# Kernel tuning notes

Measured on AMD Instinct MI355X. Metric: run time of the kernel, lower is better.

Reference implementation:

```python
import jax, jax.numpy as jnp
from jax import lax
import numpy as np


def gen_position(p, pos_decay=1.0):
    # Fixed relative-position bias: (9, p*p), neighbor order di*3+dj
    ar = jnp.arange(p, dtype=jnp.float32)
    right = jnp.broadcast_to(jnp.exp(-ar / (p / pos_decay))[None, :], (p, p))  # decays along width
    down = right.T                                                             # decays along height
    i, j = jnp.meshgrid(ar, ar, indexing='ij')
    br = jnp.exp(-(i + j) / (p / pos_decay))
    ones = jnp.ones((p, p), jnp.float32)
    merge = jnp.stack([
        jnp.rot90(br, 2), down[::-1, :], jnp.rot90(br, 1),
        right[:, ::-1], ones, right,
        jnp.rot90(br, 3), down, br,
    ], axis=0)
    return merge.reshape(9, -1)


def attention_conv(x, w_qkv, b_qkv, head_w, window_size, num_heads):
    b, c, h, w = x.shape
    p = window_size // 3
    pad_h = (p * (1 + h // p) - h) % p
    pad_w = (p * (1 + w // p) - w) % p
    xp = jnp.pad(x, ((0, 0), (0, 0), (p + pad_h, p), (p + pad_w, p)), mode='reflect')
    Hp, Wp = xp.shape[2], xp.shape[3]
    nH, nW = Hp // p - 2, Wp // p - 2  # == number of unfold windows (stride p, size 3p)
    # Non-overlapping p x p tiles; each window = 3x3 grid of adjacent tiles.
    tiles = xp.reshape(b, c, nH + 2, p, nW + 2, p).transpose(0, 2, 4, 1, 3, 5)  # [b,nH+2,nW+2,c,p,p]
    neigh = jnp.stack([tiles[:, di:di + nH, dj:dj + nW]
                       for di in range(3) for dj in range(3)], axis=3)  # [b,nH,nW,9,c,p,p]
    L = c * p * p
    pp = p * p
    xw = neigh.reshape(b * nH * nW, 9, L)
    qkv = xw @ w_qkv.T + b_qkv                                  # [N,9,nh*3*L]
    qkv = qkv.reshape(-1, 9, num_heads, 3, c, pp).transpose(0, 2, 4, 3, 1, 5)  # [N,nh,C,3,9,pp]
    q, k, v = qkv[:, :, :, 0], qkv[:, :, :, 1], qkv[:, :, :, 2]  # each [N,nh,C,9,pp]
    bias = gen_position(p)                                       # [9,pp]
    core_q = q[:, :, :, 4, :]                                    # center patch query [N,nh,C,pp]
    score = jnp.einsum('nhcp,nhckp->nhck', core_q, k * bias) / jnp.sqrt(jnp.float32(L))
    attn = jax.nn.softmax(score, axis=-1)                        # over 9 neighbors
    out = jnp.einsum('nhck,nhckp->nhcp', attn, v).reshape(-1, num_heads, L)
    out = jnp.einsum('h,nhd->nd', head_w[0], out)                # head mixing [N,L]
    out = out.reshape(b, nH, nW, c, p, p).transpose(0, 3, 1, 4, 2, 5).reshape(b, c, nH * p, nW * p)
    return out[:, :, pad_h:, pad_w:]


def setup_inputs() -> dict:
    key = jax.random.key(0)
    ks = jax.random.split(key, 8)
    B, C, H, W = 4, 3, 256, 256
    x = jax.random.uniform(ks[0], (B, C, H, W), dtype=jnp.float32)
    # conv3: window 3, p=1, heads 6, L=3 ; conv6: window 6, p=2, heads 4, L=12 ; conv9: window 9, p=3, heads 2, L=27
    w3_qkv = jax.random.normal(ks[1], (6 * 3 * 3, 3), jnp.float32) * 0.2
    b3_qkv = jnp.zeros((6 * 3 * 3,), jnp.float32)
    hw3 = jnp.full((1, 6), 1.0 / 6.0, jnp.float32)
    w6_qkv = jax.random.normal(ks[2], (4 * 3 * 12, 12), jnp.float32) * 0.1
    b6_qkv = jnp.zeros((4 * 3 * 12,), jnp.float32)
    hw6 = jnp.full((1, 4), 1.0 / 4.0, jnp.float32)
    w9_qkv = jax.random.normal(ks[3], (2 * 3 * 27, 27), jnp.float32) * 0.07
    b9_qkv = jnp.zeros((2 * 3 * 27,), jnp.float32)
    hw9 = jnp.full((1, 2), 1.0 / 2.0, jnp.float32)
    conv0_w = jax.random.normal(ks[4], (3, 9, 5, 5), jnp.float32) * 0.05
    conv0_b = jnp.zeros((3,), jnp.float32)
    return {"x": x, "w3_qkv": w3_qkv, "b3_qkv": b3_qkv, "hw3": hw3,
            "w6_qkv": w6_qkv, "b6_qkv": b6_qkv, "hw6": hw6,
            "w9_qkv": w9_qkv, "b9_qkv": b9_qkv, "hw9": hw9,
            "conv0_w": conv0_w, "conv0_b": conv0_b}


def reference(x, w3_qkv, b3_qkv, hw3, w6_qkv, b6_qkv, hw6,
              w9_qkv, b9_qkv, hw9, conv0_w, conv0_b):
    b, c, h, w = x.shape
    # global prior: softmax over size-1 dim (== ones), then global max pool
    gavg = jnp.mean((1.0 - x).reshape(b, c, -1), axis=-1, keepdims=True)       # [b,c,1]
    x_g = jax.nn.softmax(gavg, axis=-1)[..., None]                             # [b,c,1,1]
    x_g = jnp.max((x * x_g).reshape(b, 1, -1), axis=-1, keepdims=True)[..., None]  # [b,1,1,1]
    x3 = attention_conv(x,  w3_qkv, b3_qkv, hw3, 3, 6)
    x6 = attention_conv(x3, w6_qkv, b6_qkv, hw6, 6, 4)
    x9 = attention_conv(x6, w9_qkv, b9_qkv, hw9, 9, 2)
    cat = jnp.concatenate([x9, x6, x3], axis=1)                                # [b,9,h,w]
    x0 = jax.nn.relu(lax.conv_general_dilated(cat, conv0_w, (1, 1), ((2, 2), (2, 2)),
                                              dimension_numbers=('NCHW', 'OIHW', 'NCHW'))
                     + conv0_b[None, :, None, None])
    return jax.nn.relu(x * x0 + (x_g - x0))
```

## Files before the change

kernel.cpp:

```cpp
#include <hip/hip_runtime.h>
#include <math.h>

__device__ __forceinline__ int refl256(int t) {
    t = t < 0 ? -t : t;
    return t > 255 ? 510 - t : t;
}

__global__ __launch_bounds__(256)
void attn_p1v(const float* __restrict__ x, const float* __restrict__ w,
              const float* __restrict__ bq, const float* __restrict__ hw,
              float* __restrict__ out, float* __restrict__ pmax)
{
    int t = blockIdx.x * 256 + threadIdx.x;
    int xx = t & 255, yp = (t >> 8) & 127, bb = t >> 15;
    int y0 = yp * 2;
    const float* xb = x + bb * 196608;
    int rs[4], cs[3];
#pragma unroll
    for (int dr = 0; dr < 4; ++dr) rs[dr] = refl256(y0 + dr - 1) << 8;
#pragma unroll
    for (int dc = 0; dc < 3; ++dc) cs[dc] = refl256(xx + dc - 1);
    float xw[4][3][3];
#pragma unroll
    for (int dr = 0; dr < 4; ++dr)
#pragma unroll
        for (int dc = 0; dc < 3; ++dc)
#pragma unroll
            for (int c = 0; c < 3; ++c)
                xw[dr][dc][c] = xb[c * 65536 + rs[dr] + cs[dc]];

    {
        float bm = 0.f;
#pragma unroll
        for (int c = 0; c < 3; ++c)
            bm = fmaxf(bm, fmaxf(xw[1][1][c], xw[2][1][c]));
#pragma unroll
        for (int off = 32; off > 0; off >>= 1)
            bm = fmaxf(bm, __shfl_down(bm, off, 64));
        __shared__ float sm[4];
        int lane = threadIdx.x & 63, wid = threadIdx.x >> 6;
        if (lane == 0) sm[wid] = bm;
        __syncthreads();
        if (threadIdx.x == 0)
            pmax[blockIdx.x] = fmaxf(fmaxf(sm[0], sm[1]), fmaxf(sm[2], sm[3]));
    }

    float ov0[3] = {0.f, 0.f, 0.f}, ov1[3] = {0.f, 0.f, 0.f};
    const float scl = 0.57735026919f;
#pragma unroll 1
    for (int h = 0; h < 6; ++h) {
        float hwh = hw[h];
#pragma unroll
        for (int cc = 0; cc < 3; ++cc) {
            int oq = 9 * h + cc, ok = oq + 3, oV = oq + 6;
            float wq0 = w[oq * 3], wq1 = w[oq * 3 + 1], wq2 = w[oq * 3 + 2];
            float wk0 = w[ok * 3], wk1 = w[ok * 3 + 1], wk2 = w[ok * 3 + 2];
            float wv0 = w[oV * 3], wv1 = w[oV * 3 + 1], wv2 = w[oV * 3 + 2];
            float bk = bq[ok], bv = bq[oV];
            float kp[12], vp[12];
#pragma unroll
            for (int pos = 0; pos < 12; ++pos) {
                const float* xv = xw[pos / 3][pos % 3];
                kp[pos] = fmaf(xv[0], wk0, fmaf(xv[1], wk1, fmaf(xv[2], wk2, bk)));
                vp[pos] = fmaf(xv[0], wv0, fmaf(xv[1], wv1, fmaf(xv[2], wv2, bv)));
            }
            float q0 = fmaf(xw[1][1][0], wq0, fmaf(xw[1][1][1], wq1, fmaf(xw[1][1][2], wq2, bq[oq]))) * scl;
            float q1 = fmaf(xw[2][1][0], wq0, fmaf(xw[2][1][1], wq1, fmaf(xw[2][1][2], wq2, bq[oq]))) * scl;
            float se0 = 0.f, ac0 = 0.f, se1 = 0.f, ac1 = 0.f;
#pragma unroll
            for (int j = 0; j < 9; ++j) {
                float e0 = __expf(q0 * kp[j]);
                se0 += e0; ac0 = fmaf(e0, vp[j], ac0);
                float e1 = __expf(q1 * kp[3 + j]);
                se1 += e1; ac1 = fmaf(e1, vp[3 + j], ac1);
            }
            ov0[cc] = fmaf(hwh, ac0 / se0, ov0[cc]);
            ov1[cc] = fmaf(hwh, ac1 / se1, ov1[cc]);
        }
    }
    int pix = (y0 << 8) + xx;
    float* ob = out + bb * 196608;
#pragma unroll
    for (int cc = 0; cc < 3; ++cc) {
        ob[cc * 65536 + pix] = ov0[cc];
        ob[cc * 65536 + pix + 256] = ov1[cc];
    }
}

template<int P, int NH, int NWIN, int OFS, int GSU, int NCH>
__global__ __launch_bounds__(64 * NCH)
void proj2_pk(const float* __restrict__ x, const float* __restrict__ w,
              const float* __restrict__ bq, float* __restrict__ kv)
{
    constexpr int PP = P * P, L = 3 * PP, NO = NH * 9 * PP, NG = NO / GSU;
    constexpr int CPG = NG / NCH;
    constexpr int NT = NWIN + 2, T4 = 4 * NT * NT;
    constexpr int LR = (L & 1) ? L : L + 1;
    __shared__ float s_x[64 * LR];
    const int tid = threadIdx.y * 64 + threadIdx.x;
    const int t0 = blockIdx.x * 64;
    for (int idx = tid; idx < 64 * L; idx += 64 * NCH) {
        int lane = idx & 63, l = idx >> 6;
        int t = t0 + lane;
        if (t < T4) {
            int bb = t / (NT * NT), rr = t - bb * NT * NT;
            int ty = rr / NT, tx = rr - ty * NT;
            int c = l / PP, pos = l - c * PP;
            int i = pos / P, j = pos - i * P;
            int pr = refl256(ty * P + i - OFS);
            int pc = refl256(tx * P + j - OFS);
            s_x[lane * LR + l] = x[bb * 196608 + c * 65536 + (pr << 8) + pc];
        }
    }
    __syncthreads();
    const int t = t0 + threadIdx.x;
    if (t >= T4) return;
    const int chunk = __builtin_amdgcn_readfirstlane((int)threadIdx.y);
    float xw[L];
#pragma unroll
    for (int l = 0; l < L; ++l) xw[l] = s_x[threadIdx.x * LR + l];
    float4* dst = (float4*)kv + t + (size_t)chunk * CPG * T4;
#pragma unroll 1
    for (int g = 0; g < CPG; ++g) {
        int go = (chunk * CPG + g) * GSU;
        float acc[GSU];
#pragma unroll
        for (int e = 0; e < GSU; ++e) acc[e] = bq[go + e];
#pragma unroll
        for (int l = 0; l < L; ++l) {
            float xv = xw[l];
#pragma unroll
            for (int e = 0; e < GSU; ++e)
                acc[e] = fmaf(xv, w[(go + e) * L + l], acc[e]);
        }
        float4 o4;
        o4.x = acc[0];
        o4.y = acc[1];
        o4.z = acc[2];
        o4.w = (GSU == 4) ? acc[GSU - 1] : 0.f;
        dst[(size_t)g * T4] = o4;
    }
}

template<int P, int NH, int NWIN, int OFS, int GSU>
__global__ __launch_bounds__(256)
void attn2_pk(const float* __restrict__ kv, const float* __restrict__ hw,
              float* __restrict__ out)
{
    constexpr int PP = P * P, NT = NWIN + 2, T4 = 4 * NT * NT, PAD = OFS - P;
    constexpr int NGP = (PP + GSU - 1) / GSU;
    constexpr float SCL = (P == 2) ? 0.28867513459481287f : 0.19245008972987526f;
    __shared__ float s_bias[9 * PP];
    int tid = threadIdx.x;
    if (tid < 9 * PP) {
        int j = tid / PP, pos = tid - j * PP;
        int i = pos / P, jj = pos - i * P;
        int di = j / 3, dj = j - di * 3;
        float er = (di == 0) ? (float)(P - 1 - i) : (di == 2 ? (float)i : 0.f);
        float ec = (dj == 0) ? (float)(P - 1 - jj) : (dj == 2 ? (float)jj : 0.f);
        s_bias[tid] = __expf(-(er + ec) / (float)P);
    }
    __syncthreads();
    int wlin = blockIdx.x * 256 + tid;
    if (wlin >= 4 * NWIN * NWIN) return;
    int c = blockIdx.y;
    int bb = wlin / (NWIN * NWIN); int rr = wlin - bb * NWIN * NWIN;
    int yy = rr / NWIN, xx = rr - yy * NWIN;
    int tbase = bb * NT * NT + yy * NT + xx;
    int tn[9];
#pragma unroll
    for (int di = 0; di < 3; ++di)
#pragma unroll
        for (int dj = 0; dj < 3; ++dj) tn[di * 3 + dj] = tbase + di * NT + dj;
    const float4* kv4 = (const float4*)kv;
    float oa[PP];
#pragma unroll
    for (int e = 0; e < PP; ++e) oa[e] = 0.f;
#pragma unroll 1
    for (int h = 0; h < NH; ++h) {
        int oq = ((h * 3 + 0) * 3 + c) * PP;
        int ok = ((h * 3 + 1) * 3 + c) * PP;
        int ov = ((h * 3 + 2) * 3 + c) * PP;
        int gq = oq / GSU, gk = ok / GSU, gv = ov / GSU;
        float q[PP];
#pragma unroll
        for (int u = 0; u < NGP; ++u) {
            float4 t4 = kv4[(size_t)(gq + u) * T4 + tn[4]];
            float g4[4] = {t4.x, t4.y, t4.z, t4.w};
#pragma unroll
            for (int e = 0; e < GSU; ++e) q[u * GSU + e] = g4[e];
        }
        float sc[9];
#pragma unroll
        for (int j = 0; j < 9; ++j) {
            float s = 0.f;
#pragma unroll
            for (int u = 0; u < NGP; ++u) {
                float4 t4 = kv4[(size_t)(gk + u) * T4 + tn[j]];
                float g4[4] = {t4.x, t4.y, t4.z, t4.w};
#pragma unroll
                for (int e = 0; e < GSU; ++e) {
                    int Pp = u * GSU + e;
                    s = fmaf(q[Pp] * g4[e], s_bias[j * PP + Pp], s);
                }
            }
            sc[j] = s * SCL;
        }
        float se = 0.f;
#pragma unroll
        for (int j = 0; j < 9; ++j) { sc[j] = __expf(sc[j]); se += sc[j]; }
        float tmp[PP];
#pragma unroll
        for (int e = 0; e < PP; ++e) tmp[e] = 0.f;
#pragma unroll
        for (int j = 0; j < 9; ++j) {
#pragma unroll
            for (int u = 0; u < NGP; ++u) {
                float4 t4 = kv4[(size_t)(gv + u) * T4 + tn[j]];
                float g4[4] = {t4.x, t4.y, t4.z, t4.w};
#pragma unroll
                for (int e = 0; e < GSU; ++e)
                    tmp[u * GSU + e] = fmaf(sc[j], g4[e], tmp[u * GSU + e]);
            }
        }
        float f = hw[h] / se;
#pragma unroll
        for (int e = 0; e < PP; ++e) oa[e] = fmaf(f, tmp[e], oa[e]);
    }
    float* ob = out + (bb * 3 + c) * 65536;
#pragma unroll
    for (int i = 0; i < P; ++i) {
        int r = yy * P + i - PAD;
        if (PAD && r < 0) continue;
#pragma unroll
        for (int jj = 0; jj < P; ++jj) {
            int col = xx * P + jj - PAD;
            if (PAD && col < 0) continue;
            ob[(r << 8) + col] = oa[i * P + jj];
        }
    }
}

__global__ __launch_bounds__(256)
void conv_finalv(const float* __restrict__ x, const float* __restrict__ x9,
                 const float* __restrict__ x6, const float* __restrict__ x3,
                 const float* __restrict__ cw, const float* __restrict__ cb,
                 const float* __restrict__ pmax, float* __restrict__ out)
{
    int tid = threadIdx.x;
    int bb = blockIdx.x >> 6;
    __shared__ float red[128];
    __shared__ float s_g;
    if (tid < 128) red[tid] = pmax[bb * 128 + tid];
    __syncthreads();
    if (tid < 64) {
        float v = fmaxf(red[tid], red[tid + 64]);
#pragma unroll
        for (int off = 32; off > 0; off >>= 1)
            v = fmaxf(v, __shfl_down(v, off, 64));
        if (tid == 0) s_g = v;
    }
    __syncthreads();

    int gid = blockIdx.x * 256 + tid;
    int xq = (gid & 63) << 2, r = (gid >> 6) & 255;
    float a[3][4];
#pragma unroll
    for (int oc = 0; oc < 3; ++oc) {
        float b = cb[oc];
#pragma unroll
        for (int p = 0; p < 4; ++p) a[oc][p] = b;
    }
#pragma unroll 1
    for (int s = 0; s < 3; ++s) {
        const float* bp = (s == 0 ? x9 : (s == 1 ? x6 : x3)) + bb * 196608;
#pragma unroll 1
        for (int c2 = 0; c2 < 3; ++c2) {
            const float* pl = bp + c2 * 65536;
            const float* wp = cw + (s * 3 + c2) * 25;
#pragma unroll
            for (int ky = 0; ky < 5; ++ky) {
                int rr = r + ky - 2;
                if ((unsigned)rr >= 256u) continue;
                const float* row = pl + (rr << 8);
                float cv[8];
                cv[0] = (xq >= 2) ? row[xq - 2] : 0.f;
                cv[1] = (xq >= 1) ? row[xq - 1] : 0.f;
                float4 m4 = *(const float4*)(row + xq);
                cv[2] = m4.x; cv[3] = m4.y; cv[4] = m4.z; cv[5] = m4.w;
                cv[6] = (xq + 4 < 256) ? row[xq + 4] : 0.f;
                cv[7] = (xq + 5 < 256) ? row[xq + 5] : 0.f;
#pragma unroll
                for (int kx = 0; kx < 5; ++kx) {
                    float w0 = wp[ky * 5 + kx];
                    float w1 = wp[225 + ky * 5 + kx];
                    float w2 = wp[450 + ky * 5 + kx];
#pragma unroll
                    for (int p = 0; p < 4; ++p) {
                        float v = cv[kx + p];
                        a[0][p] = fmaf(v, w0, a[0][p]);
                        a[1][p] = fmaf(v, w1, a[1][p]);
                        a[2][p] = fmaf(v, w2, a[2][p]);
                    }
                }
            }
        }
    }
    float g = s_g;
    int pix = (r << 8) + xq;
    const float* xb = x + bb * 196608;
    float* ob = out + bb * 196608;
#pragma unroll
    for (int oc = 0; oc < 3; ++oc) {
        float4 xv = *(const float4*)(xb + oc * 65536 + pix);
        float4 o4;
        float x0;
        x0 = fmaxf(a[oc][0], 0.f); o4.x = fmaxf(xv.x * x0 + g - x0, 0.f);
        x0 = fmaxf(a[oc][1], 0.f); o4.y = fmaxf(xv.y * x0 + g - x0, 0.f);
        x0 = fmaxf(a[oc][2], 0.f); o4.z = fmaxf(xv.z * x0 + g - x0, 0.f);
        x0 = fmaxf(a[oc][3], 0.f); o4.w = fmaxf(xv.w * x0 + g - x0, 0.f);
        *(float4*)(ob + oc * 65536 + pix) = o4;
    }
}

extern "C" void kernel_launch(void* const* d_in, const int* in_sizes, int n_in,
                              void* d_out, int out_size, void* d_ws, size_t ws_size,
                              hipStream_t stream)
{
    const float* x   = (const float*)d_in[0];
    const float* w3  = (const float*)d_in[1];
    const float* b3  = (const float*)d_in[2];
    const float* hw3 = (const float*)d_in[3];
    const float* w6  = (const float*)d_in[4];
    const float* b6  = (const float*)d_in[5];
    const float* hw6 = (const float*)d_in[6];
    const float* w9  = (const float*)d_in[7];
    const float* b9  = (const float*)d_in[8];
    const float* hw9 = (const float*)d_in[9];
    const float* cw  = (const float*)d_in[10];
    const float* cb  = (const float*)d_in[11];

    float* ws   = (float*)d_ws;
    float* x3b  = ws;
    float* x6b  = ws + 786432;
    float* x9b  = ws + 1572864;
    float* pmax = ws + 2359296;
    float* kvb  = ws + 2359808;
    float* out  = (float*)d_out;

    attn_p1v<<<512, 256, 0, stream>>>(x, w3, b3, hw3, x3b, pmax);

    proj2_pk<2, 4, 128, 2, 4, 6><<<1057, dim3(64, 6), 0, stream>>>(x3b, w6, b6, kvb);
    attn2_pk<2, 4, 128, 2, 4><<<dim3(256, 3), 256, 0, stream>>>(kvb, hw6, x6b);
    proj2_pk<3, 2, 86, 5, 3, 9><<<484, dim3(64, 9), 0, stream>>>(x6b, w9, b9, kvb);
    attn2_pk<3, 2, 86, 5, 3><<<dim3(116, 3), 256, 0, stream>>>(kvb, hw9, x9b);

    conv_finalv<<<256, 256, 0, stream>>>(x, x9b, x6b, x3b, cw, cb, pmax, out);
}
```

Measured before the change: 178.2 us.

## Drop shared staging in projection, compute bias inline, halve conv pixels per thread

The projection kernel no longer stages the input patch through shared memory with a block barrier. Each thread now reads its own reflected patch straight from global memory, and the NCH row-threads of a block issue the same loads redundantly. The attention kernel computes the positional bias from a small table of decay powers held in registers, which removes the shared buffer and its barrier. The final conv kernel handles two pixels per thread instead of four, doubling the grid for more parallelism at the cost of more overlapping loads per output.

```diff
diff --git a/kernel.cpp b/kernel.cpp
--- a/kernel.cpp
+++ b/kernel.cpp
@@ -89,36 +89,30 @@
 
 template<int P, int NH, int NWIN, int OFS, int GSU, int NCH>
 __global__ __launch_bounds__(64 * NCH)
-void proj2_pk(const float* __restrict__ x, const float* __restrict__ w,
+void proj3_pk(const float* __restrict__ x, const float* __restrict__ w,
               const float* __restrict__ bq, float* __restrict__ kv)
 {
     constexpr int PP = P * P, L = 3 * PP, NO = NH * 9 * PP, NG = NO / GSU;
     constexpr int CPG = NG / NCH;
     constexpr int NT = NWIN + 2, T4 = 4 * NT * NT;
-    constexpr int LR = (L & 1) ? L : L + 1;
-    __shared__ float s_x[64 * LR];
-    const int tid = threadIdx.y * 64 + threadIdx.x;
-    const int t0 = blockIdx.x * 64;
-    for (int idx = tid; idx < 64 * L; idx += 64 * NCH) {
-        int lane = idx & 63, l = idx >> 6;
-        int t = t0 + lane;
-        if (t < T4) {
-            int bb = t / (NT * NT), rr = t - bb * NT * NT;
-            int ty = rr / NT, tx = rr - ty * NT;
-            int c = l / PP, pos = l - c * PP;
-            int i = pos / P, j = pos - i * P;
-            int pr = refl256(ty * P + i - OFS);
-            int pc = refl256(tx * P + j - OFS);
-            s_x[lane * LR + l] = x[bb * 196608 + c * 65536 + (pr << 8) + pc];
-        }
-    }
-    __syncthreads();
-    const int t = t0 + threadIdx.x;
+    int t = blockIdx.x * 64 + threadIdx.x;
     if (t >= T4) return;
     const int chunk = __builtin_amdgcn_readfirstlane((int)threadIdx.y);
+    int bb = t / (NT * NT), rr = t - bb * NT * NT;
+    int ty = rr / NT, tx = rr - ty * NT;
+    const float* xb = x + bb * 196608;
     float xw[L];
 #pragma unroll
-    for (int l = 0; l < L; ++l) xw[l] = s_x[threadIdx.x * LR + l];
+    for (int i = 0; i < P; ++i) {
+        int pr = refl256(ty * P + i - OFS) << 8;
+#pragma unroll
+        for (int j = 0; j < P; ++j) {
+            int pc = refl256(tx * P + j - OFS);
+#pragma unroll
+            for (int c = 0; c < 3; ++c)
+                xw[c * PP + i * P + j] = xb[c * 65536 + pr + pc];
+        }
+    }
     float4* dst = (float4*)kv + t + (size_t)chunk * CPG * T4;
 #pragma unroll 1
     for (int g = 0; g < CPG; ++g) {
@@ -150,17 +144,13 @@
     constexpr int PP = P * P, NT = NWIN + 2, T4 = 4 * NT * NT, PAD = OFS - P;
     constexpr int NGP = (PP + GSU - 1) / GSU;
     constexpr float SCL = (P == 2) ? 0.28867513459481287f : 0.19245008972987526f;
-    __shared__ float s_bias[9 * PP];
+    constexpr float DD  = (P == 2) ? 0.6065306597126334f : 0.7165313105737893f;
+    float dpw[2 * P - 1];
+    dpw[0] = 1.f;
+#pragma unroll
+    for (int k = 1; k < 2 * P - 1; ++k) dpw[k] = dpw[k - 1] * DD;
+
     int tid = threadIdx.x;
-    if (tid < 9 * PP) {
-        int j = tid / PP, pos = tid - j * PP;
-        int i = pos / P, jj = pos - i * P;
-        int di = j / 3, dj = j - di * 3;
-        float er = (di == 0) ? (float)(P - 1 - i) : (di == 2 ? (float)i : 0.f);
-        float ec = (dj == 0) ? (float)(P - 1 - jj) : (dj == 2 ? (float)jj : 0.f);
-        s_bias[tid] = __expf(-(er + ec) / (float)P);
-    }
-    __syncthreads();
     int wlin = blockIdx.x * 256 + tid;
     if (wlin >= 4 * NWIN * NWIN) return;
     int c = blockIdx.y;
@@ -193,6 +183,7 @@
         float sc[9];
 #pragma unroll
         for (int j = 0; j < 9; ++j) {
+            int di = j / 3, dj = j - di * 3;
             float s = 0.f;
 #pragma unroll
             for (int u = 0; u < NGP; ++u) {
@@ -201,7 +192,10 @@
 #pragma unroll
                 for (int e = 0; e < GSU; ++e) {
                     int Pp = u * GSU + e;
-                    s = fmaf(q[Pp] * g4[e], s_bias[j * PP + Pp], s);
+                    int i = Pp / P, jj = Pp - i * P;
+                    int er = (di == 0) ? (P - 1 - i) : (di == 2 ? i : 0);
+                    int ec = (dj == 0) ? (P - 1 - jj) : (dj == 2 ? jj : 0);
+                    s = fmaf(q[Pp] * g4[e], dpw[er + ec], s);
                 }
             }
             sc[j] = s * SCL;
@@ -242,13 +236,13 @@
 }
 
 __global__ __launch_bounds__(256)
-void conv_finalv(const float* __restrict__ x, const float* __restrict__ x9,
-                 const float* __restrict__ x6, const float* __restrict__ x3,
-                 const float* __restrict__ cw, const float* __restrict__ cb,
-                 const float* __restrict__ pmax, float* __restrict__ out)
+void conv_finalv2(const float* __restrict__ x, const float* __restrict__ x9,
+                  const float* __restrict__ x6, const float* __restrict__ x3,
+                  const float* __restrict__ cw, const float* __restrict__ cb,
+                  const float* __restrict__ pmax, float* __restrict__ out)
 {
     int tid = threadIdx.x;
-    int bb = blockIdx.x >> 6;
+    int bb = blockIdx.x >> 7;
     __shared__ float red[128];
     __shared__ float s_g;
     if (tid < 128) red[tid] = pmax[bb * 128 + tid];
@@ -263,13 +257,12 @@
     __syncthreads();
 
     int gid = blockIdx.x * 256 + tid;
-    int xq = (gid & 63) << 2, r = (gid >> 6) & 255;
-    float a[3][4];
+    int xp = (gid & 127) << 1, r = (gid >> 7) & 255;
+    float a[3][2];
 #pragma unroll
     for (int oc = 0; oc < 3; ++oc) {
         float b = cb[oc];
-#pragma unroll
-        for (int p = 0; p < 4; ++p) a[oc][p] = b;
+        a[oc][0] = b; a[oc][1] = b;
     }
 #pragma unroll 1
     for (int s = 0; s < 3; ++s) {
@@ -283,43 +276,37 @@
                 int rr = r + ky - 2;
                 if ((unsigned)rr >= 256u) continue;
                 const float* row = pl + (rr << 8);
-                float cv[8];
-                cv[0] = (xq >= 2) ? row[xq - 2] : 0.f;
-                cv[1] = (xq >= 1) ? row[xq - 1] : 0.f;
-                float4 m4 = *(const float4*)(row + xq);
-                cv[2] = m4.x; cv[3] = m4.y; cv[4] = m4.z; cv[5] = m4.w;
-                cv[6] = (xq + 4 < 256) ? row[xq + 4] : 0.f;
-                cv[7] = (xq + 5 < 256) ? row[xq + 5] : 0.f;
+                float2 va = (xp >= 2) ? *(const float2*)(row + xp - 2)
+                                      : make_float2(0.f, 0.f);
+                float2 vb = *(const float2*)(row + xp);
+                float2 vc = (xp + 2 < 256) ? *(const float2*)(row + xp + 2)
+                                           : make_float2(0.f, 0.f);
+                float cv[6] = {va.x, va.y, vb.x, vb.y, vc.x, vc.y};
 #pragma unroll
                 for (int kx = 0; kx < 5; ++kx) {
                     float w0 = wp[ky * 5 + kx];
                     float w1 = wp[225 + ky * 5 + kx];
                     float w2 = wp[450 + ky * 5 + kx];
-#pragma unroll
-                    for (int p = 0; p < 4; ++p) {
-                        float v = cv[kx + p];
-                        a[0][p] = fmaf(v, w0, a[0][p]);
-                        a[1][p] = fmaf(v, w1, a[1][p]);
-                        a[2][p] = fmaf(v, w2, a[2][p]);
-                    }
+                    float v0 = cv[kx], v1 = cv[kx + 1];
+                    a[0][0] = fmaf(v0, w0, a[0][0]); a[0][1] = fmaf(v1, w0, a[0][1]);
+                    a[1][0] = fmaf(v0, w1, a[1][0]); a[1][1] = fmaf(v1, w1, a[1][1]);
+                    a[2][0] = fmaf(v0, w2, a[2][0]); a[2][1] = fmaf(v1, w2, a[2][1]);
                 }
             }
         }
     }
     float g = s_g;
-    int pix = (r << 8) + xq;
+    int pix = (r << 8) + xp;
     const float* xb = x + bb * 196608;
     float* ob = out + bb * 196608;
 #pragma unroll
     for (int oc = 0; oc < 3; ++oc) {
-        float4 xv = *(const float4*)(xb + oc * 65536 + pix);
-        float4 o4;
+        float2 xv = *(const float2*)(xb + oc * 65536 + pix);
+        float2 o2;
         float x0;
-        x0 = fmaxf(a[oc][0], 0.f); o4.x = fmaxf(xv.x * x0 + g - x0, 0.f);
-        x0 = fmaxf(a[oc][1], 0.f); o4.y = fmaxf(xv.y * x0 + g - x0, 0.f);
-        x0 = fmaxf(a[oc][2], 0.f); o4.z = fmaxf(xv.z * x0 + g - x0, 0.f);
-        x0 = fmaxf(a[oc][3], 0.f); o4.w = fmaxf(xv.w * x0 + g - x0, 0.f);
-        *(float4*)(ob + oc * 65536 + pix) = o4;
+        x0 = fmaxf(a[oc][0], 0.f); o2.x = fmaxf(xv.x * x0 + g - x0, 0.f);
+        x0 = fmaxf(a[oc][1], 0.f); o2.y = fmaxf(xv.y * x0 + g - x0, 0.f);
+        *(float2*)(ob + oc * 65536 + pix) = o2;
     }
 }
 
@@ -350,10 +337,10 @@
 
     attn_p1v<<<512, 256, 0, stream>>>(x, w3, b3, hw3, x3b, pmax);
 
-    proj2_pk<2, 4, 128, 2, 4, 6><<<1057, dim3(64, 6), 0, stream>>>(x3b, w6, b6, kvb);
+    proj3_pk<2, 4, 128, 2, 4, 6><<<1057, dim3(64, 6), 0, stream>>>(x3b, w6, b6, kvb);
     attn2_pk<2, 4, 128, 2, 4><<<dim3(256, 3), 256, 0, stream>>>(kvb, hw6, x6b);
-    proj2_pk<3, 2, 86, 5, 3, 9><<<484, dim3(64, 9), 0, stream>>>(x6b, w9, b9, kvb);
+    proj3_pk<3, 2, 86, 5, 3, 9><<<484, dim3(64, 9), 0, stream>>>(x6b, w9, b9, kvb);
     attn2_pk<3, 2, 86, 5, 3><<<dim3(116, 3), 256, 0, stream>>>(kvb, hw9, x9b);
 
-    conv_finalv<<<256, 256, 0, stream>>>(x, x9b, x6b, x3b, cw, cb, pmax, out);
-}
+    conv_finalv2<<<512, 256, 0, stream>>>(x, x9b, x6b, x3b, cw, cb, pmax, out);
+}
```

Measured after the change: 171.5 us. 3.7% less time.
